# Optimization experiments

Hardware: AMD Instinct MI355X
Metric: run time of the kernel (lower is better)

The kernel has to match this reference:

```python
import jax, jax.numpy as jnp
import numpy as np
from jax import lax

N = 8192
TARGET_COMPONENTS = 1.0
TARGET_CYCLES = 0.0
WEIGHT = 1.0
THRESH_SHIFT = 2.0


def setup_inputs() -> dict:
    key = jax.random.key(0)
    x = jax.random.normal(key, (N, N), dtype=jnp.float32)
    # symmetrize so directed DFS traversal == undirected connectivity,
    # then shift so adj > 0 is sparse (realistic learned graph structure)
    adj = (x + x.T) * 0.5 - THRESH_SHIFT
    return {"adj": adj}


def _count_components(adj):
    """Connected components via min-label propagation (parallel equivalent
    of the serial DFS in the torch module for a symmetric adjacency)."""
    n = adj.shape[0]
    pos = adj > 0  # [n, n] bool edge mask
    labels0 = jnp.arange(n, dtype=jnp.int32)

    def body(state):
        labels, _ = state
        # min label among neighbors (n = sentinel for non-edges)
        neigh_min = jnp.min(jnp.where(pos, labels[None, :], jnp.int32(n)), axis=1)
        new_labels = jnp.minimum(labels, neigh_min)
        return new_labels, jnp.any(new_labels != labels)

    labels, _ = lax.while_loop(lambda s: s[1], body,
                               (labels0, jnp.array(True)))
    # exactly one node per component keeps its own (minimal) index
    return jnp.sum((labels == labels0).astype(jnp.int32))


def reference(adj):
    n = adj.shape[0]
    n_comp = _count_components(adj).astype(jnp.float32)
    n_edges = (jnp.sum((adj > 0).astype(jnp.int32)) // 2).astype(jnp.float32)
    betti_1 = n_edges - jnp.float32(n) + n_comp           # Betti-1 estimate
    n_cycles = jnp.maximum(jnp.float32(0.0), betti_1)
    component_loss = (n_comp - TARGET_COMPONENTS) ** 2
    cycle_loss = (n_cycles - TARGET_CYCLES) ** 2
    return WEIGHT * (component_loss + cycle_loss)
```

## Files before the change

### kernel.cpp

```cpp
#include <hip/hip_runtime.h>


#define NN 8192
#define SCAN_LDS_CAP 2048

__global__ __launch_bounds__(64) void init_kernel(int* counters) {
    if (threadIdx.x < 2) counters[threadIdx.x] = 0;
}

__global__ __launch_bounds__(256) void scan_kernel(const float* __restrict__ adj,
                                                   int* __restrict__ counters,
                                                   unsigned int* __restrict__ ebuf,
                                                   int cap) {
    __shared__ int lds_n;
    __shared__ int lds_base;
    __shared__ unsigned int lds_e[SCAN_LDS_CAP];
    if (threadIdx.x == 0) lds_n = 0;
    __syncthreads();

    int b = blockIdx.x;
    int ra = b;
    int rb = NN - 1 - b;
    int nfa = (ra + 4) >> 2;
    int nfb = (rb + 4) >> 2;
    int tot = nfa + nfb;

    int t = threadIdx.x;
    int c1 = 0;

    float4 v[9];
    int   rr[9];
    int   gg[9];
    bool  ok[9];

    #pragma unroll
    for (int k = 0; k < 9; ++k) {
        int vg = t + (k << 8);
        ok[k] = vg < tot;
        bool inA = vg < nfa;
        int r = inA ? ra : rb;
        int g = inA ? vg : vg - nfa;
        rr[k] = r;
        gg[k] = g;
        if (ok[k]) v[k] = ((const float4*)(adj + (size_t)r * NN))[g];
    }

    #pragma unroll
    for (int k = 0; k < 9; ++k) {
        if (!ok[k]) continue;
        int r  = rr[k];
        int j0 = gg[k] << 2;
        float vv[4] = {v[k].x, v[k].y, v[k].z, v[k].w};
        #pragma unroll
        for (int c = 0; c < 4; ++c) {
            int j = j0 + c;
            bool pos = vv[c] > 0.0f;
            if (pos && j < r) {
                int kk = atomicAdd(&lds_n, 1);
                unsigned int e = ((unsigned)r << 13) | (unsigned)j;
                if (kk < SCAN_LDS_CAP) lds_e[kk] = e;
                else {
                    int gk = atomicAdd(counters, 1);
                    if (gk < cap) ebuf[gk] = e;
                }
            }
            c1 += (pos && j == r) ? 1 : 0;
        }
    }

    #pragma unroll
    for (int off = 32; off > 0; off >>= 1) c1 += __shfl_down(c1, off, 64);
    if ((t & 63) == 0 && c1) atomicAdd(counters + 1, c1);

    __syncthreads();
    int n = lds_n < SCAN_LDS_CAP ? lds_n : SCAN_LDS_CAP;
    if (t == 0) lds_base = atomicAdd(counters, n);
    __syncthreads();
    int base = lds_base;
    for (int k = t; k < n; k += 256) {
        int idx = base + k;
        if (idx < cap) ebuf[idx] = lds_e[k];
    }
}

__global__ __launch_bounds__(1024) void label_final_kernel(
        const unsigned int* __restrict__ ebuf,
        const int* __restrict__ counters,
        int cap, float* __restrict__ out) {
    __shared__ int lab[NN];
    __shared__ int changed;
    __shared__ int wsum[16];
    int tid = threadIdx.x;
    for (int i = tid; i < NN; i += 1024) lab[i] = i;
    __syncthreads();

    int total_lower = counters[0];
    int m = total_lower < cap ? total_lower : cap;

    for (;;) {
        if (tid == 0) changed = 0;
        __syncthreads();

        for (int base = tid; base < m; base += 8192) {
            unsigned int e[8];
            bool val[8];
            #pragma unroll
            for (int q = 0; q < 8; ++q) {
                int idx = base + (q << 10);
                val[q] = idx < m;
                if (val[q]) e[q] = ebuf[idx];
            }
            #pragma unroll
            for (int q = 0; q < 8; ++q) {
                if (!val[q]) continue;
                int r = (int)(e[q] >> 13);
                int j = (int)(e[q] & (NN - 1));
                int lr = lab[r];
                int lj = lab[j];
                if (lj < lr) {
                    int old = atomicMin(&lab[r], lj);
                    if (lj < old) changed = 1;
                } else if (lr < lj) {
                    int old = atomicMin(&lab[j], lr);
                    if (lr < old) changed = 1;
                }
            }
        }
        __syncthreads();

        #pragma unroll
        for (int s = 0; s < 2; ++s) {
            for (int i = tid; i < NN; i += 1024) {
                int l = lab[i];
                int ll = lab[l];
                if (ll < l) { lab[i] = ll; changed = 1; }
            }
        }
        __syncthreads();

        if (changed == 0) break;
        __syncthreads();
    }

    int cnt = 0;
    for (int i = tid; i < NN; i += 1024) cnt += (lab[i] == i) ? 1 : 0;
    #pragma unroll
    for (int off = 32; off > 0; off >>= 1) cnt += __shfl_down(cnt, off, 64);
    if ((tid & 63) == 0) wsum[tid >> 6] = cnt;
    __syncthreads();
    if (tid == 0) {
        int roots = 0;
        #pragma unroll
        for (int w = 0; w < 16; ++w) roots += wsum[w];
        long long total = 2LL * (long long)total_lower + (long long)counters[1];
        long long n_edges_i = total >> 1;
        double n_comp = (double)roots;
        double comp_loss = (n_comp - 1.0) * (n_comp - 1.0);
        double betti = (double)n_edges_i - (double)NN + n_comp;
        double cyc = betti > 0.0 ? betti : 0.0;
        out[0] = (float)(comp_loss + cyc * cyc);
    }
}

extern "C" void kernel_launch(void* const* d_in, const int* in_sizes, int n_in,
                              void* d_out, int out_size, void* d_ws, size_t ws_size,
                              hipStream_t stream) {
    const float* adj = (const float*)d_in[0];
    int* ws = (int*)d_ws;
    int* counters = ws;
    unsigned int* ebuf = (unsigned int*)(ws + 2);
    long long cap_ll = (long long)(ws_size / 4) - 2;
    int cap = cap_ll > 0x7fffffff ? 0x7fffffff : (cap_ll < 0 ? 0 : (int)cap_ll);
    float* out = (float*)d_out;

    init_kernel<<<1, 64, 0, stream>>>(counters);
    scan_kernel<<<NN / 2, 256, 0, stream>>>(adj, counters, ebuf, cap);
    label_final_kernel<<<1, 1024, 0, stream>>>(ebuf, counters, cap, out);
}
```

Measured before the change: 404.0 us.

## Cache edge list in registers across label-propagation iterations

The single-block labeling kernel now loads each thread's share of the edge list into a large register array once, then reuses it on every propagation iteration instead of re-reading the buffer from global memory each pass. Block size drops from 1024 to 512 threads to make room for 160 edges per thread, with a global-memory fallback loop for any overflow. Pointer-jumping passes per iteration increase from two to three. The cost is heavy register pressure and fewer threads issuing LDS atomics, which may reduce parallelism.

```diff
diff --git a/kernel.cpp b/kernel.cpp
--- a/kernel.cpp
+++ b/kernel.cpp
@@ -3,6 +3,9 @@
 
 #define NN 8192
 #define SCAN_LDS_CAP 2048
+#define LBL_THREADS 512
+#define EPT 160
+#define REGCAP (LBL_THREADS * EPT)
 
 __global__ __launch_bounds__(64) void init_kernel(int* counters) {
     if (threadIdx.x < 2) counters[threadIdx.x] = 0;
@@ -83,54 +86,60 @@
     }
 }
 
-__global__ __launch_bounds__(1024) void label_final_kernel(
+__global__ __launch_bounds__(LBL_THREADS) void label_final_kernel(
         const unsigned int* __restrict__ ebuf,
         const int* __restrict__ counters,
         int cap, float* __restrict__ out) {
     __shared__ int lab[NN];
     __shared__ int changed;
-    __shared__ int wsum[16];
+    __shared__ int wsum[LBL_THREADS / 64];
     int tid = threadIdx.x;
-    for (int i = tid; i < NN; i += 1024) lab[i] = i;
-    __syncthreads();
+    for (int i = tid; i < NN; i += LBL_THREADS) lab[i] = i;
 
     int total_lower = counters[0];
     int m = total_lower < cap ? total_lower : cap;
+
+    unsigned int e[EPT];
+    #pragma unroll
+    for (int q = 0; q < EPT; ++q) {
+        int idx = tid + q * LBL_THREADS;
+        e[q] = (idx < m) ? ebuf[idx] : 0u;
+    }
+    __syncthreads();
 
     for (;;) {
         if (tid == 0) changed = 0;
         __syncthreads();
 
-        for (int base = tid; base < m; base += 8192) {
-            unsigned int e[8];
-            bool val[8];
-            #pragma unroll
-            for (int q = 0; q < 8; ++q) {
-                int idx = base + (q << 10);
-                val[q] = idx < m;
-                if (val[q]) e[q] = ebuf[idx];
+        #pragma unroll
+        for (int q = 0; q < EPT; ++q) {
+            int r = (int)(e[q] >> 13);
+            int j = (int)(e[q] & (NN - 1));
+            int lr = lab[r];
+            int lj = lab[j];
+            if (lj < lr) {
+                if (atomicMin(&lab[r], lj) > lj) changed = 1;
+            } else if (lr < lj) {
+                if (atomicMin(&lab[j], lr) > lr) changed = 1;
             }
-            #pragma unroll
-            for (int q = 0; q < 8; ++q) {
-                if (!val[q]) continue;
-                int r = (int)(e[q] >> 13);
-                int j = (int)(e[q] & (NN - 1));
-                int lr = lab[r];
-                int lj = lab[j];
-                if (lj < lr) {
-                    int old = atomicMin(&lab[r], lj);
-                    if (lj < old) changed = 1;
-                } else if (lr < lj) {
-                    int old = atomicMin(&lab[j], lr);
-                    if (lr < old) changed = 1;
-                }
+        }
+        for (int idx = REGCAP + tid; idx < m; idx += LBL_THREADS) {
+            unsigned int eg = ebuf[idx];
+            int r = (int)(eg >> 13);
+            int j = (int)(eg & (NN - 1));
+            int lr = lab[r];
+            int lj = lab[j];
+            if (lj < lr) {
+                if (atomicMin(&lab[r], lj) > lj) changed = 1;
+            } else if (lr < lj) {
+                if (atomicMin(&lab[j], lr) > lr) changed = 1;
             }
         }
         __syncthreads();
 
         #pragma unroll
-        for (int s = 0; s < 2; ++s) {
-            for (int i = tid; i < NN; i += 1024) {
+        for (int s = 0; s < 3; ++s) {
+            for (int i = tid; i < NN; i += LBL_THREADS) {
                 int l = lab[i];
                 int ll = lab[l];
                 if (ll < l) { lab[i] = ll; changed = 1; }
@@ -143,7 +152,7 @@
     }
 
     int cnt = 0;
-    for (int i = tid; i < NN; i += 1024) cnt += (lab[i] == i) ? 1 : 0;
+    for (int i = tid; i < NN; i += LBL_THREADS) cnt += (lab[i] == i) ? 1 : 0;
     #pragma unroll
     for (int off = 32; off > 0; off >>= 1) cnt += __shfl_down(cnt, off, 64);
     if ((tid & 63) == 0) wsum[tid >> 6] = cnt;
@@ -151,7 +160,7 @@
     if (tid == 0) {
         int roots = 0;
         #pragma unroll
-        for (int w = 0; w < 16; ++w) roots += wsum[w];
+        for (int w = 0; w < LBL_THREADS / 64; ++w) roots += wsum[w];
         long long total = 2LL * (long long)total_lower + (long long)counters[1];
         long long n_edges_i = total >> 1;
         double n_comp = (double)roots;
@@ -175,5 +184,5 @@
 
     init_kernel<<<1, 64, 0, stream>>>(counters);
     scan_kernel<<<NN / 2, 256, 0, stream>>>(adj, counters, ebuf, cap);
-    label_final_kernel<<<1, 1024, 0, stream>>>(ebuf, counters, cap, out);
+    label_final_kernel<<<1, LBL_THREADS, 0, stream>>>(ebuf, counters, cap, out);
 }
```

Measured after the change: 471.9 us. 16.8% more time.
